# Kernel optimization log

Measured on AMD Instinct MI355X. Metric: run time of the kernel, lower is better.

Reference implementation:

```python
import jax, jax.numpy as jnp
import numpy as np

D_MODEL = 1024
N_HEADS = 16
DH = (D_MODEL // N_HEADS) // 2  # depth // 2 = 32
B, S = 4, 2048


def setup_inputs() -> dict:
    key = jax.random.key(0)
    ks = jax.random.split(key, 8)
    scale_in = 1.0
    q = jax.random.normal(ks[0], (B, S, D_MODEL), dtype=jnp.float32)
    k = jax.random.normal(ks[1], (B, S, D_MODEL), dtype=jnp.float32)
    v = jax.random.normal(ks[2], (B, S, D_MODEL), dtype=jnp.float32)
    # Per-head projection weights stacked over the head axis (glorot-ish init)
    w_std = (2.0 / (D_MODEL + DH)) ** 0.5
    Wq = jax.random.normal(ks[3], (N_HEADS, D_MODEL, DH), dtype=jnp.float32) * w_std
    Wk = jax.random.normal(ks[4], (N_HEADS, D_MODEL, DH), dtype=jnp.float32) * w_std
    Wv = jax.random.normal(ks[5], (N_HEADS, D_MODEL, DH), dtype=jnp.float32) * w_std
    wo_std = (2.0 / (N_HEADS * DH + D_MODEL)) ** 0.5
    Wo = jax.random.normal(ks[6], (N_HEADS * DH, D_MODEL), dtype=jnp.float32) * wo_std
    return {"q": q, "k": k, "v": v, "Wq": Wq, "Wk": Wk, "Wv": Wv, "Wo": Wo}


def reference(q, k, v, Wq, Wk, Wv, Wo):
    # NOTE: source scales by d_model**-0.5 (not head_dim**-0.5)
    scale = D_MODEL ** (-0.5)
    Q = jnp.einsum("bsd,hde->bhse", q, Wq)   # [B,H,S,DH]
    K = jnp.einsum("btd,hde->bhte", k, Wk)
    V = jnp.einsum("btd,hde->bhte", v, Wv)
    attn = jnp.einsum("bhse,bhte->bhst", Q, K) * scale  # [B,H,S,S]
    attn = jax.nn.softmax(attn, axis=-1)
    x = jnp.einsum("bhst,bhte->bhse", attn, V)  # [B,H,S,DH]
    # concat heads along feature dim (head order = concat order in source)
    x = jnp.transpose(x, (0, 2, 1, 3)).reshape(q.shape[0], q.shape[1], N_HEADS * DH)
    return x @ Wo  # [B,S,D_MODEL]; dropout is identity (training=False)
```

## Files before the change

kernel.cpp:

```cpp
#include <hip/hip_runtime.h>
#include <hip/hip_bf16.h>

typedef __attribute__((ext_vector_type(8))) short short8;
typedef __attribute__((ext_vector_type(4))) float f32x4;
typedef __attribute__((ext_vector_type(4))) float fv4;
typedef __attribute__((ext_vector_type(4))) unsigned int u32x4;

#define MFMA16(a, b, c) __builtin_amdgcn_mfma_f32_16x16x32_bf16((a), (b), (c), 0, 0, 0)
#define SBAR() __builtin_amdgcn_sched_barrier(0)

typedef const __attribute__((address_space(1))) unsigned int gu32;
typedef __attribute__((address_space(3))) unsigned int lu32;

__device__ __forceinline__ short f2b(float f) {
  unsigned int x = __builtin_bit_cast(unsigned int, f);
  x += 0x7fffu + ((x >> 16) & 1u);
  return (short)(x >> 16);
}

__device__ __forceinline__ unsigned int cvtpk(float lo, float hi) {
  unsigned int r;
  asm("v_cvt_pk_bf16_f32 %0, %1, %2" : "=v"(r) : "v"(lo), "v"(hi));
  return r;
}

#define hexp2(x) __builtin_amdgcn_exp2f(x)

__global__ void prep_weights(const float* __restrict__ Wq, const float* __restrict__ Wk,
                             const float* __restrict__ Wv, const float* __restrict__ Wo,
                             short* __restrict__ WqT, short* __restrict__ WkT,
                             short* __restrict__ WvT, short* __restrict__ WoT) {
  const float SC2 = 0.045084220027780106f;
  int idx = blockIdx.x * 256 + threadIdx.x;
  if (idx < 3 * 512 * 1024) {
    int wsel = idx >> 19;
    int rem = idx & ((1 << 19) - 1);
    int n = rem >> 10;
    int d = rem & 1023;
    const float* W = (wsel == 0) ? Wq : ((wsel == 1) ? Wk : Wv);
    short* WT = (wsel == 0) ? WqT : ((wsel == 1) ? WkT : WvT);
    float v = W[(n >> 5) * (1024 * 32) + d * 32 + (n & 31)];
    if (wsel == 0) v *= SC2;
    WT[n * 1024 + d] = f2b(v);
  } else {
    int idx2 = idx - 3 * 512 * 1024;
    int n = idx2 >> 9;
    int kk = idx2 & 511;
    WoT[n * 512 + kk] = f2b(Wo[kk * 1024 + n]);
  }
}

__global__ __launch_bounds__(256, 3) void proj_gemm(
    const float* __restrict__ q, const float* __restrict__ k, const float* __restrict__ v,
    const short* __restrict__ WqT, const short* __restrict__ WkT, const short* __restrict__ WvT,
    short* __restrict__ Qb, short* __restrict__ Kb, short* __restrict__ Vtb) {
  __shared__ char smem[32768];
  const int tid = threadIdx.x;
  const int lane = tid & 63;
  const int w = tid >> 6;
  const int l15 = lane & 15, g = lane >> 4;
  const int wm = (w >> 1) * 64, wn = (w & 1) * 64;
  const int id = blockIdx.x;
  const int bm = id & 63;
  const int r = id >> 6;
  const int bn = r & 3;
  const int z = r >> 2;
  const float* A = (z == 0) ? q : ((z == 1) ? k : v);
  const short* BT = (z == 0) ? WqT : ((z == 1) ? WkT : WvT);
  const int bm0 = bm * 128, bn0 = bn * 128;

  const int arow = w * 32 + (lane >> 1);
  const int ahalf = lane & 1;
  const int aswz = (arow >> 1) & 3;
  const float* Ag = A + (size_t)(bm0 + arow) * 1024 + ahalf * 16;
  const int aw_off0 = arow * 64 + (((2 * ahalf) ^ aswz) * 16);
  const int aw_off1 = arow * 64 + (((2 * ahalf + 1) ^ aswz) * 16);

  const int brow0 = w * 32 + (lane >> 2);
  const int brow1 = brow0 + 16;
  const short* Bg0 = BT + (size_t)(bn0 + brow0) * 1024 + 8 * ((lane & 3) ^ ((brow0 >> 1) & 3));
  const short* Bg1 = BT + (size_t)(bn0 + brow1) * 1024 + 8 * ((lane & 3) ^ ((brow1 >> 1) & 3));

  f32x4 zf = {0.f, 0.f, 0.f, 0.f};
  f32x4 acc[4][4];
#pragma unroll
  for (int a = 0; a < 4; ++a)
#pragma unroll
    for (int bq = 0; bq < 4; ++bq) acc[a][bq] = zf;

  fv4 fa0, fa1, fa2, fa3;
#define GLOADA(k0)                          \
  fa0 = *(const fv4*)(Ag + (k0));           \
  fa1 = *(const fv4*)(Ag + (k0) + 4);       \
  fa2 = *(const fv4*)(Ag + (k0) + 8);       \
  fa3 = *(const fv4*)(Ag + (k0) + 12);

#define WRITEA(aoff)                                                  \
  {                                                                   \
    u32x4 wv0, wv1;                                                   \
    wv0[0] = cvtpk(fa0[0], fa0[1]);                                   \
    wv0[1] = cvtpk(fa0[2], fa0[3]);                                   \
    wv0[2] = cvtpk(fa1[0], fa1[1]);                                   \
    wv0[3] = cvtpk(fa1[2], fa1[3]);                                   \
    wv1[0] = cvtpk(fa2[0], fa2[1]);                                   \
    wv1[1] = cvtpk(fa2[2], fa2[3]);                                   \
    wv1[2] = cvtpk(fa3[0], fa3[1]);                                   \
    wv1[3] = cvtpk(fa3[2], fa3[3]);                                   \
    *(short8*)(smem + (aoff) + aw_off0) = __builtin_bit_cast(short8, wv0); \
    *(short8*)(smem + (aoff) + aw_off1) = __builtin_bit_cast(short8, wv1); \
  }

#define STAGEB(boff, k0)                                                      \
  {                                                                           \
    __builtin_amdgcn_global_load_lds((gu32*)(Bg0 + (k0)),                     \
                                     (lu32*)(smem + (boff) + w * 2048), 16, 0, 0); \
    __builtin_amdgcn_global_load_lds((gu32*)(Bg1 + (k0)),                     \
                                     (lu32*)(smem + (boff) + w * 2048 + 1024), 16, 0, 0); \
  }

#define COMPUTE(aoff, boff)                                                    \
  {                                                                            \
    short8 af[4], bfr[4];                                                      \
    _Pragma("unroll") for (int mf = 0; mf < 4; ++mf) {                         \
      int ar = wm + mf * 16 + l15;                                             \
      af[mf] = *(const short8*)(smem + (aoff) + ar * 64 +                      \
                                ((g ^ ((ar >> 1) & 3)) * 16));                 \
    }                                                                          \
    _Pragma("unroll") for (int nf = 0; nf < 4; ++nf) {                         \
      int br = wn + nf * 16 + l15;                                             \
      bfr[nf] = *(const short8*)(smem + (boff) + br * 64 +                     \
                                 ((g ^ ((br >> 1) & 3)) * 16));                \
    }                                                                          \
    _Pragma("unroll") for (int mf = 0; mf < 4; ++mf)                           \
        _Pragma("unroll") for (int nf = 0; nf < 4; ++nf)                       \
            acc[mf][nf] = MFMA16(af[mf], bfr[nf], acc[mf][nf]);                \
  }

  GLOADA(0);
  STAGEB(16384, 0);
  WRITEA(0);
  __syncthreads();

  for (int k0 = 0; k0 < 1024; k0 += 32) {
    const int cur = (k0 >> 5) & 1;
    const int nxt = cur ^ 1;
    const int acur = cur * 8192, anxt = nxt * 8192;
    const int bcur = 16384 + cur * 8192, bnxt = 16384 + nxt * 8192;
    if (k0 + 32 < 1024) {
      GLOADA(k0 + 32);
      STAGEB(bnxt, k0 + 32);
    }
    SBAR();
    COMPUTE(acur, bcur);
    SBAR();
    if (k0 + 32 < 1024) WRITEA(anxt);
    __syncthreads();
  }
#undef GLOADA
#undef WRITEA
#undef STAGEB
#undef COMPUTE

#pragma unroll
  for (int mf = 0; mf < 4; ++mf)
#pragma unroll
    for (int nf = 0; nf < 4; ++nf)
#pragma unroll
      for (int i = 0; i < 4; ++i) {
        int row = bm0 + wm + mf * 16 + g * 4 + i;
        int col = bn0 + wn + nf * 16 + l15;
        int bb = row >> 11, ss = row & 2047;
        int hh = col >> 5, ee = col & 31;
        short val = f2b(acc[mf][nf][i]);
        if (z == 2)
          Vtb[((size_t)(bb * 16 + hh) * 32 + ee) * 2048 + ss] = val;
        else if (z == 1)
          Kb[((size_t)(bb * 16 + hh) * 2048 + ss) * 32 + ee] = val;
        else
          Qb[((size_t)(bb * 16 + hh) * 2048 + ss) * 32 + ee] = val;
      }
}

__global__ __launch_bounds__(256, 2) void out_gemm(const short* __restrict__ X,
                                                   const short* __restrict__ WoT,
                                                   float* __restrict__ out) {
  __shared__ char smem[32768];
  const int tid = threadIdx.x;
  const int lane = tid & 63;
  const int w = tid >> 6;
  const int l15 = lane & 15, g = lane >> 4;
  const int wm = (w >> 1) * 64, wn = (w & 1) * 64;
  const int id = blockIdx.x;
  const int bm0 = (id & 63) * 128, bn0 = (id >> 6) * 128;

  const int row0 = w * 32 + (lane >> 2);
  const int row1 = row0 + 16;
  const int sl = lane & 3;
  const short* Ag0 = X + (size_t)(bm0 + row0) * 512 + 8 * (sl ^ ((row0 >> 1) & 3));
  const short* Ag1 = X + (size_t)(bm0 + row1) * 512 + 8 * (sl ^ ((row1 >> 1) & 3));
  const short* Bg0 = WoT + (size_t)(bn0 + row0) * 512 + 8 * (sl ^ ((row0 >> 1) & 3));
  const short* Bg1 = WoT + (size_t)(bn0 + row1) * 512 + 8 * (sl ^ ((row1 >> 1) & 3));

  f32x4 zf = {0.f, 0.f, 0.f, 0.f};
  f32x4 acc[4][4];
#pragma unroll
  for (int a = 0; a < 4; ++a)
#pragma unroll
    for (int bq = 0; bq < 4; ++bq) acc[a][bq] = zf;

#define STAGE(aoff, boff, k0)                                                     \
  {                                                                               \
    __builtin_amdgcn_global_load_lds((gu32*)(Ag0 + (k0)),                         \
                                     (lu32*)(smem + (aoff) + w * 2048), 16, 0, 0); \
    __builtin_amdgcn_global_load_lds((gu32*)(Ag1 + (k0)),                         \
                                     (lu32*)(smem + (aoff) + w * 2048 + 1024), 16, 0, 0); \
    __builtin_amdgcn_global_load_lds((gu32*)(Bg0 + (k0)),                         \
                                     (lu32*)(smem + (boff) + w * 2048), 16, 0, 0); \
    __builtin_amdgcn_global_load_lds((gu32*)(Bg1 + (k0)),                         \
                                     (lu32*)(smem + (boff) + w * 2048 + 1024), 16, 0, 0); \
  }

#define COMPUTE(aoff, boff)                                                    \
  {                                                                            \
    short8 af[4], bfr[4];                                                      \
    _Pragma("unroll") for (int mf = 0; mf < 4; ++mf) {                         \
      int ar = wm + mf * 16 + l15;                                             \
      af[mf] = *(const short8*)(smem + (aoff) + ar * 64 +                      \
                                ((g ^ ((ar >> 1) & 3)) * 16));                 \
    }                                                                          \
    _Pragma("unroll") for (int nf = 0; nf < 4; ++nf) {                         \
      int br = wn + nf * 16 + l15;                                             \
      bfr[nf] = *(const short8*)(smem + (boff) + br * 64 +                     \
                                 ((g ^ ((br >> 1) & 3)) * 16));                \
    }                                                                          \
    _Pragma("unroll") for (int mf = 0; mf < 4; ++mf)                           \
        _Pragma("unroll") for (int nf = 0; nf < 4; ++nf)                       \
            acc[mf][nf] = MFMA16(af[mf], bfr[nf], acc[mf][nf]);                \
  }

  STAGE(0, 16384, 0);
  __syncthreads();
  for (int k0 = 0; k0 < 512; k0 += 32) {
    const int cur = (k0 >> 5) & 1;
    const int nxt = cur ^ 1;
    if (k0 + 32 < 512) {
      STAGE(nxt * 8192, 16384 + nxt * 8192, k0 + 32);
    }
    SBAR();
    COMPUTE(cur * 8192, 16384 + cur * 8192);
    SBAR();
    __syncthreads();
  }
#undef STAGE
#undef COMPUTE

#pragma unroll
  for (int mf = 0; mf < 4; ++mf)
#pragma unroll
    for (int nf = 0; nf < 4; ++nf)
#pragma unroll
      for (int i = 0; i < 4; ++i) {
        int row = bm0 + wm + mf * 16 + g * 4 + i;
        int col = bn0 + wn + nf * 16 + l15;
        out[(size_t)row * 1024 + col] = acc[mf][nf][i];
      }
}

__device__ __forceinline__ void qk_half(short8 k0, short8 k1, short8 k2, short8 k3,
                                        short8 qf, const f32x4& zf,
                                        short8& pf0, short8& pf1) {
  f32x4 s0 = MFMA16(k0, qf, zf);
  f32x4 s1 = MFMA16(k1, qf, zf);
  f32x4 s2 = MFMA16(k2, qf, zf);
  f32x4 s3 = MFMA16(k3, qf, zf);
#pragma unroll
  for (int i = 0; i < 4; ++i) {
    s0[i] = hexp2(s0[i]);
    s1[i] = hexp2(s1[i]);
    s2[i] = hexp2(s2[i]);
    s3[i] = hexp2(s3[i]);
  }
  u32x4 w0, w1;
  w0[0] = cvtpk(s0[0], s0[1]);
  w0[1] = cvtpk(s0[2], s0[3]);
  w0[2] = cvtpk(s1[0], s1[1]);
  w0[3] = cvtpk(s1[2], s1[3]);
  w1[0] = cvtpk(s2[0], s2[1]);
  w1[1] = cvtpk(s2[2], s2[3]);
  w1[2] = cvtpk(s3[0], s3[1]);
  w1[3] = cvtpk(s3[2], s3[3]);
  pf0 = __builtin_bit_cast(short8, w0);
  pf1 = __builtin_bit_cast(short8, w1);
}

__global__ __launch_bounds__(256, 4) void attn(const short* __restrict__ Qb,
                                               const short* __restrict__ Kb,
                                               const short* __restrict__ Vtb,
                                               short* __restrict__ X) {
  __shared__ short KV[2][2][2048];
  const int tid = threadIdx.x;
  const int lane = tid & 63;
  const int w = tid >> 6;
  const int l15 = lane & 15, g = lane >> 4;
  const int id = blockIdx.x;
  const int bh = id & 63;
  const int qblk = id >> 6;
  const int bb = bh >> 4, hh = bh & 15;
  const int q0 = qblk * 128 + w * 32;

  const short* Qp = Qb + ((size_t)bh * 2048 + q0) * 32;
  const short* Kp = Kb + (size_t)bh * 2048 * 32;
  const short* Vp = Vtb + (size_t)bh * 32 * 2048;

  short8 qfA = *(const short8*)(Qp + l15 * 32 + g * 8);
  short8 qfB = *(const short8*)(Qp + (16 + l15) * 32 + g * 8);

  const int kbase = 8 * (l15 >> 2) + (l15 & 3);
  const int koff = (w & 1) * 4 + (w >> 1) * 32;
  const int vrow = (w >> 1) * 16;
  const int vcol = (w & 1) * 32;
  const short* Ksrc0 = Kp + (size_t)(kbase + koff) * 32 + g * 8;
  const short* Vsrc0 = Vp + (size_t)(l15 + vrow) * 2048 + vcol + g * 8;

  f32x4 zf = {0.f, 0.f, 0.f, 0.f};
  f32x4 o_loA = zf, o_hiA = zf, o_loB = zf, o_hiB = zf;
  f32x4 accLA = zf, accLB = zf;
  u32x4 ones_u = {0x3F803F80u, 0x3F803F80u, 0x3F803F80u, 0x3F803F80u};
  const short8 ones = __builtin_bit_cast(short8, ones_u);

#define STAGE(b, t0)                                                        \
  {                                                                         \
    __builtin_amdgcn_global_load_lds((gu32*)(Ksrc0 + (size_t)(t0) * 32),    \
                                     (lu32*)&KV[b][0][w * 512], 16, 0, 0);  \
    __builtin_amdgcn_global_load_lds((gu32*)(Vsrc0 + (t0)),                 \
                                     (lu32*)&KV[b][1][w * 512], 16, 0, 0);  \
  }

#define BODY(b)                                                       \
  {                                                                   \
    short8 k0 = *(const short8*)(&KV[b][0][0 * 512 + lane * 8]);      \
    short8 k1 = *(const short8*)(&KV[b][0][1 * 512 + lane * 8]);      \
    short8 k2 = *(const short8*)(&KV[b][0][2 * 512 + lane * 8]);      \
    short8 k3 = *(const short8*)(&KV[b][0][3 * 512 + lane * 8]);      \
    short8 vlo0 = *(const short8*)(&KV[b][1][0 * 512 + lane * 8]);    \
    short8 vlo1 = *(const short8*)(&KV[b][1][1 * 512 + lane * 8]);    \
    short8 vhi0 = *(const short8*)(&KV[b][1][2 * 512 + lane * 8]);    \
    short8 vhi1 = *(const short8*)(&KV[b][1][3 * 512 + lane * 8]);    \
    short8 pfA0, pfA1, pfB0, pfB1;                                    \
    qk_half(k0, k1, k2, k3, qfA, zf, pfA0, pfA1);                     \
    qk_half(k0, k1, k2, k3, qfB, zf, pfB0, pfB1);                     \
    __builtin_amdgcn_s_setprio(1);                                    \
    accLA = MFMA16(pfA0, ones, accLA);                                \
    accLA = MFMA16(pfA1, ones, accLA);                                \
    accLB = MFMA16(pfB0, ones, accLB);                                \
    accLB = MFMA16(pfB1, ones, accLB);                                \
    o_loA = MFMA16(pfA0, vlo0, o_loA);                                \
    o_loA = MFMA16(pfA1, vlo1, o_loA);                                \
    o_hiA = MFMA16(pfA0, vhi0, o_hiA);                                \
    o_hiA = MFMA16(pfA1, vhi1, o_hiA);                                \
    o_loB = MFMA16(pfB0, vlo0, o_loB);                                \
    o_loB = MFMA16(pfB1, vlo1, o_loB);                                \
    o_hiB = MFMA16(pfB0, vhi0, o_hiB);                                \
    o_hiB = MFMA16(pfB1, vhi1, o_hiB);                                \
    __builtin_amdgcn_s_setprio(0);                                    \
  }

  STAGE(0, 0);
  __syncthreads();
  for (int t0 = 0; t0 < 2048; t0 += 128) {
    STAGE(1, t0 + 64);
    BODY(0);
    __syncthreads();
    if (t0 + 128 < 2048) {
      STAGE(0, t0 + 128);
    }
    BODY(1);
    __syncthreads();
  }
#undef STAGE
#undef BODY

#pragma unroll
  for (int i = 0; i < 4; ++i) {
    float invA = 1.0f / accLA[i];
    float invB = 1.0f / accLB[i];
    int ssA = q0 + 4 * g + i;
    size_t baseA = ((size_t)bb * 2048 + ssA) * 512 + hh * 32;
    X[baseA + l15] = f2b(o_loA[i] * invA);
    X[baseA + 16 + l15] = f2b(o_hiA[i] * invA);
    size_t baseB = baseA + (size_t)16 * 512;
    X[baseB + l15] = f2b(o_loB[i] * invB);
    X[baseB + 16 + l15] = f2b(o_hiB[i] * invB);
  }
}

extern "C" void kernel_launch(void* const* d_in, const int* in_sizes, int n_in,
                              void* d_out, int out_size, void* d_ws, size_t ws_size,
                              hipStream_t stream) {
  const float* q = (const float*)d_in[0];
  const float* k = (const float*)d_in[1];
  const float* v = (const float*)d_in[2];
  const float* Wq = (const float*)d_in[3];
  const float* Wk = (const float*)d_in[4];
  const float* Wv = (const float*)d_in[5];
  const float* Wo = (const float*)d_in[6];

  char* ws = (char*)d_ws;
  const size_t MB = 1u << 20;
  short* WqT = (short*)(ws + 0 * MB);
  short* WkT = (short*)(ws + 1 * MB);
  short* WvT = (short*)(ws + 2 * MB);
  short* WoT = (short*)(ws + 3 * MB);
  short* Qb  = (short*)(ws + 4 * MB);
  short* Kb  = (short*)(ws + 12 * MB);
  short* Vtb = (short*)(ws + 20 * MB);
  short* Xb  = (short*)(ws + 28 * MB);

  prep_weights<<<8192, 256, 0, stream>>>(Wq, Wk, Wv, Wo, WqT, WkT, WvT, WoT);
  proj_gemm<<<768, 256, 0, stream>>>(q, k, v, WqT, WkT, WvT, Qb, Kb, Vtb);
  attn<<<1024, 256, 0, stream>>>(Qb, Kb, Vtb, Xb);
  out_gemm<<<512, 256, 0, stream>>>(Xb, WoT, (float*)d_out);
}
```

Baseline: 122.6 us.

## Stage fp32 activations directly to LDS and convert at fragment read

proj_gemm now loads the fp32 q/k/v tiles straight into LDS with global_load_lds, using an XOR-swizzled 128-byte row layout, and converts them to bf16 while reading MFMA fragments. This replaces the old path of loading into registers, converting, and writing to LDS. Both GEMMs also replace __syncthreads with explicit vmcnt waits plus a raw s_barrier, so the next tile's async loads overlap compute with one wait per iteration. The cost is more LDS per block (48KB in proj_gemm), twice the LDS read traffic for A, and conversion work repeated on every fragment read.

```diff
diff --git a/kernel.cpp b/kernel.cpp
--- a/kernel.cpp
+++ b/kernel.cpp
@@ -8,6 +8,7 @@
 
 #define MFMA16(a, b, c) __builtin_amdgcn_mfma_f32_16x16x32_bf16((a), (b), (c), 0, 0, 0)
 #define SBAR() __builtin_amdgcn_sched_barrier(0)
+#define RBAR() __builtin_amdgcn_s_barrier()
 
 typedef const __attribute__((address_space(1))) unsigned int gu32;
 typedef __attribute__((address_space(3))) unsigned int lu32;
@@ -52,9 +53,9 @@
 
 __global__ __launch_bounds__(256, 3) void proj_gemm(
     const float* __restrict__ q, const float* __restrict__ k, const float* __restrict__ v,
-    const short* __restrict__ WqT, const short* __restrict__ WkT, const short* __restrict__ WvT,
+    const short* __restrict__ BTall,
     short* __restrict__ Qb, short* __restrict__ Kb, short* __restrict__ Vtb) {
-  __shared__ char smem[32768];
+  __shared__ char smem[49152];
   const int tid = threadIdx.x;
   const int lane = tid & 63;
   const int w = tid >> 6;
@@ -62,24 +63,23 @@
   const int wm = (w >> 1) * 64, wn = (w & 1) * 64;
   const int id = blockIdx.x;
   const int bm = id & 63;
-  const int r = id >> 6;
-  const int bn = r & 3;
-  const int z = r >> 2;
-  const float* A = (z == 0) ? q : ((z == 1) ? k : v);
-  const short* BT = (z == 0) ? WqT : ((z == 1) ? WkT : WvT);
+  const int bn = id >> 6;
   const int bm0 = bm * 128, bn0 = bn * 128;
-
-  const int arow = w * 32 + (lane >> 1);
-  const int ahalf = lane & 1;
-  const int aswz = (arow >> 1) & 3;
-  const float* Ag = A + (size_t)(bm0 + arow) * 1024 + ahalf * 16;
-  const int aw_off0 = arow * 64 + (((2 * ahalf) ^ aswz) * 16);
-  const int aw_off1 = arow * 64 + (((2 * ahalf + 1) ^ aswz) * 16);
-
-  const int brow0 = w * 32 + (lane >> 2);
-  const int brow1 = brow0 + 16;
-  const short* Bg0 = BT + (size_t)(bn0 + brow0) * 1024 + 8 * ((lane & 3) ^ ((brow0 >> 1) & 3));
-  const short* Bg1 = BT + (size_t)(bn0 + brow1) * 1024 + 8 * ((lane & 3) ^ ((brow1 >> 1) & 3));
+  const int z = blockIdx.y;
+  (void)z;
+  const float* A = q;
+  (void)A;
+
+  const int zz = bn >> 2;
+  const int bnz = bn & 3;
+  const float* Az = (zz == 0) ? q : ((zz == 1) ? k : v);
+  const short* BT = BTall + (size_t)zz * 512 * 1024;
+  const int bn0z = bnz * 128;
+
+  const int ar = (lane >> 3);
+  const int au = lane & 7;
+  const int br = (lane >> 2);
+  const int bu = lane & 3;
 
   f32x4 zf = {0.f, 0.f, 0.f, 0.f};
   f32x4 acc[4][4];
@@ -88,77 +88,66 @@
 #pragma unroll
     for (int bq = 0; bq < 4; ++bq) acc[a][bq] = zf;
 
-  fv4 fa0, fa1, fa2, fa3;
-#define GLOADA(k0)                          \
-  fa0 = *(const fv4*)(Ag + (k0));           \
-  fa1 = *(const fv4*)(Ag + (k0) + 4);       \
-  fa2 = *(const fv4*)(Ag + (k0) + 8);       \
-  fa3 = *(const fv4*)(Ag + (k0) + 12);
-
-#define WRITEA(aoff)                                                  \
-  {                                                                   \
-    u32x4 wv0, wv1;                                                   \
-    wv0[0] = cvtpk(fa0[0], fa0[1]);                                   \
-    wv0[1] = cvtpk(fa0[2], fa0[3]);                                   \
-    wv0[2] = cvtpk(fa1[0], fa1[1]);                                   \
-    wv0[3] = cvtpk(fa1[2], fa1[3]);                                   \
-    wv1[0] = cvtpk(fa2[0], fa2[1]);                                   \
-    wv1[1] = cvtpk(fa2[2], fa2[3]);                                   \
-    wv1[2] = cvtpk(fa3[0], fa3[1]);                                   \
-    wv1[3] = cvtpk(fa3[2], fa3[3]);                                   \
-    *(short8*)(smem + (aoff) + aw_off0) = __builtin_bit_cast(short8, wv0); \
-    *(short8*)(smem + (aoff) + aw_off1) = __builtin_bit_cast(short8, wv1); \
-  }
-
-#define STAGEB(boff, k0)                                                      \
-  {                                                                           \
-    __builtin_amdgcn_global_load_lds((gu32*)(Bg0 + (k0)),                     \
-                                     (lu32*)(smem + (boff) + w * 2048), 16, 0, 0); \
-    __builtin_amdgcn_global_load_lds((gu32*)(Bg1 + (k0)),                     \
-                                     (lu32*)(smem + (boff) + w * 2048 + 1024), 16, 0, 0); \
-  }
-
-#define COMPUTE(aoff, boff)                                                    \
+#define STAGE(base, k0)                                                        \
+  {                                                                            \
+    _Pragma("unroll") for (int i = 0; i < 4; ++i) {                            \
+      int row = 32 * w + 8 * i + ar;                                           \
+      __builtin_amdgcn_global_load_lds(                                        \
+          (gu32*)(Az + (size_t)(bm0 + row) * 1024 + (k0) + 4 * (au ^ (row & 7))), \
+          (lu32*)(smem + (base) + w * 4096 + i * 1024), 16, 0, 0);             \
+    }                                                                          \
+    _Pragma("unroll") for (int i = 0; i < 2; ++i) {                            \
+      int row = 32 * w + 16 * i + br;                                          \
+      __builtin_amdgcn_global_load_lds(                                        \
+          (gu32*)(BT + (size_t)(bn0z + row) * 1024 + (k0) +                    \
+                  8 * (bu ^ ((row >> 1) & 3))),                                \
+          (lu32*)(smem + (base) + 16384 + w * 2048 + i * 1024), 16, 0, 0);     \
+    }                                                                          \
+  }
+
+#define COMPUTE(base)                                                          \
   {                                                                            \
     short8 af[4], bfr[4];                                                      \
     _Pragma("unroll") for (int mf = 0; mf < 4; ++mf) {                         \
-      int ar = wm + mf * 16 + l15;                                             \
-      af[mf] = *(const short8*)(smem + (aoff) + ar * 64 +                      \
-                                ((g ^ ((ar >> 1) & 3)) * 16));                 \
+      int row = wm + mf * 16 + l15;                                            \
+      fv4 a0 = *(const fv4*)(smem + (base) + row * 128 +                       \
+                             (((2 * g) ^ (row & 7)) * 16));                    \
+      fv4 a1 = *(const fv4*)(smem + (base) + row * 128 +                       \
+                             (((2 * g + 1) ^ (row & 7)) * 16));                \
+      u32x4 wv;                                                                \
+      wv[0] = cvtpk(a0[0], a0[1]);                                             \
+      wv[1] = cvtpk(a0[2], a0[3]);                                             \
+      wv[2] = cvtpk(a1[0], a1[1]);                                             \
+      wv[3] = cvtpk(a1[2], a1[3]);                                             \
+      af[mf] = __builtin_bit_cast(short8, wv);                                 \
     }                                                                          \
     _Pragma("unroll") for (int nf = 0; nf < 4; ++nf) {                         \
-      int br = wn + nf * 16 + l15;                                             \
-      bfr[nf] = *(const short8*)(smem + (boff) + br * 64 +                     \
-                                 ((g ^ ((br >> 1) & 3)) * 16));                \
+      int row = wn + nf * 16 + l15;                                            \
+      bfr[nf] = *(const short8*)(smem + (base) + 16384 + row * 64 +            \
+                                 ((g ^ ((row >> 1) & 3)) * 16));               \
     }                                                                          \
     _Pragma("unroll") for (int mf = 0; mf < 4; ++mf)                           \
         _Pragma("unroll") for (int nf = 0; nf < 4; ++nf)                       \
             acc[mf][nf] = MFMA16(af[mf], bfr[nf], acc[mf][nf]);                \
   }
 
-  GLOADA(0);
-  STAGEB(16384, 0);
-  WRITEA(0);
-  __syncthreads();
-
+  STAGE(0, 0);
   for (int k0 = 0; k0 < 1024; k0 += 32) {
     const int cur = (k0 >> 5) & 1;
-    const int nxt = cur ^ 1;
-    const int acur = cur * 8192, anxt = nxt * 8192;
-    const int bcur = 16384 + cur * 8192, bnxt = 16384 + nxt * 8192;
+    const int cbase = cur * 24576;
+    const int nbase = (cur ^ 1) * 24576;
     if (k0 + 32 < 1024) {
-      GLOADA(k0 + 32);
-      STAGEB(bnxt, k0 + 32);
+      STAGE(nbase, k0 + 32);
+      asm volatile("s_waitcnt vmcnt(6)" ::: "memory");
+    } else {
+      asm volatile("s_waitcnt vmcnt(0)" ::: "memory");
     }
+    RBAR();
     SBAR();
-    COMPUTE(acur, bcur);
-    SBAR();
-    if (k0 + 32 < 1024) WRITEA(anxt);
-    __syncthreads();
-  }
-#undef GLOADA
-#undef WRITEA
-#undef STAGEB
+    COMPUTE(cbase);
+    RBAR();
+  }
+#undef STAGE
 #undef COMPUTE
 
 #pragma unroll
@@ -168,13 +157,13 @@
 #pragma unroll
       for (int i = 0; i < 4; ++i) {
         int row = bm0 + wm + mf * 16 + g * 4 + i;
-        int col = bn0 + wn + nf * 16 + l15;
+        int col = bn0z + wn + nf * 16 + l15;
         int bb = row >> 11, ss = row & 2047;
         int hh = col >> 5, ee = col & 31;
         short val = f2b(acc[mf][nf][i]);
-        if (z == 2)
+        if (zz == 2)
           Vtb[((size_t)(bb * 16 + hh) * 32 + ee) * 2048 + ss] = val;
-        else if (z == 1)
+        else if (zz == 1)
           Kb[((size_t)(bb * 16 + hh) * 2048 + ss) * 32 + ee] = val;
         else
           Qb[((size_t)(bb * 16 + hh) * 2048 + ss) * 32 + ee] = val;
@@ -193,13 +182,8 @@
   const int id = blockIdx.x;
   const int bm0 = (id & 63) * 128, bn0 = (id >> 6) * 128;
 
-  const int row0 = w * 32 + (lane >> 2);
-  const int row1 = row0 + 16;
-  const int sl = lane & 3;
-  const short* Ag0 = X + (size_t)(bm0 + row0) * 512 + 8 * (sl ^ ((row0 >> 1) & 3));
-  const short* Ag1 = X + (size_t)(bm0 + row1) * 512 + 8 * (sl ^ ((row1 >> 1) & 3));
-  const short* Bg0 = WoT + (size_t)(bn0 + row0) * 512 + 8 * (sl ^ ((row0 >> 1) & 3));
-  const short* Bg1 = WoT + (size_t)(bn0 + row1) * 512 + 8 * (sl ^ ((row1 >> 1) & 3));
+  const int br = (lane >> 2);
+  const int bu = lane & 3;
 
   f32x4 zf = {0.f, 0.f, 0.f, 0.f};
   f32x4 acc[4][4];
@@ -208,48 +192,54 @@
 #pragma unroll
     for (int bq = 0; bq < 4; ++bq) acc[a][bq] = zf;
 
-#define STAGE(aoff, boff, k0)                                                     \
-  {                                                                               \
-    __builtin_amdgcn_global_load_lds((gu32*)(Ag0 + (k0)),                         \
-                                     (lu32*)(smem + (aoff) + w * 2048), 16, 0, 0); \
-    __builtin_amdgcn_global_load_lds((gu32*)(Ag1 + (k0)),                         \
-                                     (lu32*)(smem + (aoff) + w * 2048 + 1024), 16, 0, 0); \
-    __builtin_amdgcn_global_load_lds((gu32*)(Bg0 + (k0)),                         \
-                                     (lu32*)(smem + (boff) + w * 2048), 16, 0, 0); \
-    __builtin_amdgcn_global_load_lds((gu32*)(Bg1 + (k0)),                         \
-                                     (lu32*)(smem + (boff) + w * 2048 + 1024), 16, 0, 0); \
-  }
-
-#define COMPUTE(aoff, boff)                                                    \
+#define STAGE(base, k0)                                                        \
+  {                                                                            \
+    _Pragma("unroll") for (int i = 0; i < 2; ++i) {                            \
+      int row = 32 * w + 16 * i + br;                                          \
+      __builtin_amdgcn_global_load_lds(                                        \
+          (gu32*)(X + (size_t)(bm0 + row) * 512 + (k0) +                       \
+                  8 * (bu ^ ((row >> 1) & 3))),                                \
+          (lu32*)(smem + (base) + w * 2048 + i * 1024), 16, 0, 0);             \
+      __builtin_amdgcn_global_load_lds(                                        \
+          (gu32*)(WoT + (size_t)(bn0 + row) * 512 + (k0) +                     \
+                  8 * (bu ^ ((row >> 1) & 3))),                                \
+          (lu32*)(smem + (base) + 8192 + w * 2048 + i * 1024), 16, 0, 0);      \
+    }                                                                          \
+  }
+
+#define COMPUTE(base)                                                          \
   {                                                                            \
     short8 af[4], bfr[4];                                                      \
     _Pragma("unroll") for (int mf = 0; mf < 4; ++mf) {                         \
-      int ar = wm + mf * 16 + l15;                                             \
-      af[mf] = *(const short8*)(smem + (aoff) + ar * 64 +                      \
-                                ((g ^ ((ar >> 1) & 3)) * 16));                 \
+      int row = wm + mf * 16 + l15;                                            \
+      af[mf] = *(const short8*)(smem + (base) + row * 64 +                     \
+                                ((g ^ ((row >> 1) & 3)) * 16));                \
     }                                                                          \
     _Pragma("unroll") for (int nf = 0; nf < 4; ++nf) {                         \
-      int br = wn + nf * 16 + l15;                                             \
-      bfr[nf] = *(const short8*)(smem + (boff) + br * 64 +                     \
-                                 ((g ^ ((br >> 1) & 3)) * 16));                \
+      int row = wn + nf * 16 + l15;                                            \
+      bfr[nf] = *(const short8*)(smem + (base) + 8192 + row * 64 +             \
+                                 ((g ^ ((row >> 1) & 3)) * 16));               \
     }                                                                          \
     _Pragma("unroll") for (int mf = 0; mf < 4; ++mf)                           \
         _Pragma("unroll") for (int nf = 0; nf < 4; ++nf)                       \
             acc[mf][nf] = MFMA16(af[mf], bfr[nf], acc[mf][nf]);                \
   }
 
-  STAGE(0, 16384, 0);
-  __syncthreads();
+  STAGE(0, 0);
   for (int k0 = 0; k0 < 512; k0 += 32) {
     const int cur = (k0 >> 5) & 1;
-    const int nxt = cur ^ 1;
+    const int cbase = cur * 16384;
+    const int nbase = (cur ^ 1) * 16384;
     if (k0 + 32 < 512) {
-      STAGE(nxt * 8192, 16384 + nxt * 8192, k0 + 32);
+      STAGE(nbase, k0 + 32);
+      asm volatile("s_waitcnt vmcnt(4)" ::: "memory");
+    } else {
+      asm volatile("s_waitcnt vmcnt(0)" ::: "memory");
     }
+    RBAR();
     SBAR();
-    COMPUTE(cur * 8192, 16384 + cur * 8192);
-    SBAR();
-    __syncthreads();
+    COMPUTE(cbase);
+    RBAR();
   }
 #undef STAGE
 #undef COMPUTE
@@ -417,7 +407,7 @@
   short* Xb  = (short*)(ws + 28 * MB);
 
   prep_weights<<<8192, 256, 0, stream>>>(Wq, Wk, Wv, Wo, WqT, WkT, WvT, WoT);
-  proj_gemm<<<768, 256, 0, stream>>>(q, k, v, WqT, WkT, WvT, Qb, Kb, Vtb);
+  proj_gemm<<<768, 256, 0, stream>>>(q, k, v, WqT, Qb, Kb, Vtb);
   attn<<<1024, 256, 0, stream>>>(Qb, Kb, Vtb, Xb);
   out_gemm<<<512, 256, 0, stream>>>(Xb, WoT, (float*)d_out);
 }
```

After: 118.1 us. 1.04x faster.
